# Optimization experiments

Measured on AMD Instinct MI355X. Metric: run time of the kernel, lower is better.

Reference implementation:

```python
import jax, jax.numpy as jnp
import numpy as np

KERNEL_SIZE = 5
SIGMA = 2.0
HALF_K = KERNEL_SIZE // 2


def _gaussian_kernel():
    # torch: arange(-k//2+1, k//2+1) with python floor div -> [-2,...,2] for k=5
    ax = jnp.arange(-(KERNEL_SIZE // 2), KERNEL_SIZE // 2 + 1, dtype=jnp.float32)
    xx, yy = jnp.meshgrid(ax, ax, indexing='ij')
    k = jnp.exp(-(xx ** 2 + yy ** 2) / (2.0 * SIGMA ** 2))
    return k / k.sum()  # [5,5]


def setup_inputs() -> dict:
    key = jax.random.key(0)
    k1, k2 = jax.random.split(key)
    feature_map = jax.random.normal(k1, (512, 256, 256), dtype=jnp.float32)
    keypoints = jax.random.randint(k2, (4096, 2), 0, 256, dtype=jnp.int64)
    return {"feature_map": feature_map, "keypoints": keypoints}


def reference(feature_map, keypoints):
    C, H, W = feature_map.shape
    kern = _gaussian_kernel().astype(feature_map.dtype)  # [5,5]
    x = jnp.clip(keypoints[:, 0].astype(jnp.int32), HALF_K, W - HALF_K - 1)  # [N]
    y = jnp.clip(keypoints[:, 1].astype(jnp.int32), HALF_K, H - HALF_K - 1)  # [N]

    def pool_one(xi, yi):
        patch = jax.lax.dynamic_slice(
            feature_map, (0, yi - HALF_K, xi - HALF_K), (C, KERNEL_SIZE, KERNEL_SIZE)
        )  # [C,5,5]
        return jnp.einsum('chw,hw->c', patch, kern)  # [C]

    return jax.vmap(pool_one)(x, y)  # [N,C]
```

## Files before the change

kernel.cpp:

```cpp
#include <hip/hip_runtime.h>


#define NC  512
#define NH  256
#define NW  256
#define NKP 4096

#define OCT 8
#define SLICE_ROWS 36
#define STR 260

#define WS_LIST_OFF_I 16
#define WS_OUTT_OFF_B 262144

__global__ __launch_bounds__(256) void bucket_kernel(
    const int* __restrict__ kp, unsigned* __restrict__ ws_i, int n_kp)
{
    __shared__ unsigned llist[NKP];
    __shared__ int lcnt;
    const int q = blockIdx.x;
    const int t = threadIdx.x;
    if (t == 0) lcnt = 0;
    __syncthreads();

    for (int i = t; i < n_kp; i += 256) {
        int x = kp[2 * i + 0];
        int y = kp[2 * i + 1];
        x = min(max(x, 2), NW - 3);
        y = min(max(y, 2), NH - 3);
        if ((y >> 5) == q) {
            int pos = atomicAdd(&lcnt, 1);
            llist[pos] = (unsigned)i | ((unsigned)x << 12) | ((unsigned)y << 20);
        }
    }
    __syncthreads();
    const int c = lcnt;
    for (int i = t; i < c; i += 256)
        ws_i[WS_LIST_OFF_I + q * NKP + i] = llist[i];
    if (t == 0) ws_i[q] = (unsigned)c;
}

__global__ __launch_bounds__(256) void pool_kernel(
    const float* __restrict__ fm, const unsigned* __restrict__ ws_i,
    float* __restrict__ outT)
{
    __shared__ float plane[SLICE_ROWS * STR];

    const int c = blockIdx.x;
    const int q = blockIdx.y;
    const int t = threadIdx.x;
    const int ybase = q * 32 - 2;

    const float4* src = (const float4*)(fm + ((size_t)c << 16));
#pragma unroll
    for (int it = 0; it < (SLICE_ROWS * 64) / 256; ++it) {
        const int i = t + it * 256;
        const int row = i >> 6;
        const int col4 = i & 63;
        const int gr = ybase + row;
        if ((unsigned)gr < 256u) {
            float4 v = src[(gr << 6) + col4];
            *(float4*)&plane[row * STR + (col4 << 2)] = v;
        }
    }
    __syncthreads();

    const float e1 = 0.8824969025845955f;
    const float e2 = 0.6065306597126334f;
    const float s  = 2.0f * (e1 + e2) + 1.0f;
    const float inv_s2 = 1.0f / (s * s);
    const float g[5] = {e2, e1, 1.0f, e1, e2};
    float gy[5];
#pragma unroll
    for (int i = 0; i < 5; i++) gy[i] = g[i] * inv_s2;

    const int cnt = (int)ws_i[q];
    const unsigned* list = ws_i + WS_LIST_OFF_I + q * NKP;

    for (int e = t; e < cnt; e += 256) {
        const unsigned pk = list[e];
        const int n  = (int)(pk & 0xFFFu);
        const int xc = (int)((pk >> 12) & 0xFFu);
        const int yc = (int)((pk >> 20) & 0xFFu);

        const int x0 = xc - 2;
        const int r  = x0 & 3;
        const int xa = x0 - r;
        float wx[8];
#pragma unroll
        for (int i = 0; i < 8; i++)
            wx[i] = (i >= r && i < r + 5) ? g[i - r] : 0.0f;

        const int lr0 = yc - (q << 5);
        float acc = 0.0f;
#pragma unroll
        for (int dy = 0; dy < 5; dy++) {
            const float* rowp = &plane[(lr0 + dy) * STR + xa];
            float4 a = *(const float4*)rowp;
            float4 b = *(const float4*)(rowp + 4);
            acc += gy[dy] * (a.x * wx[0] + a.y * wx[1] + a.z * wx[2] + a.w * wx[3]
                           + b.x * wx[4] + b.y * wx[5] + b.z * wx[6] + b.w * wx[7]);
        }
        outT[((size_t)c << 12) + n] = acc;
    }
}

__global__ __launch_bounds__(256) void outt_kernel(
    const float* __restrict__ outT, float* __restrict__ out)
{
    __shared__ float tile[32][33];
    const int n0 = blockIdx.x * 32;
    const int c0 = blockIdx.y * 32;
    const int tx = threadIdx.x;
    const int ty = threadIdx.y;

#pragma unroll
    for (int k = 0; k < 32; k += 8)
        tile[ty + k][tx] = outT[(size_t)(c0 + ty + k) * NKP + n0 + tx];
    __syncthreads();
#pragma unroll
    for (int k = 0; k < 32; k += 8)
        out[(size_t)(n0 + ty + k) * NC + c0 + tx] = tile[tx][ty + k];
}

__global__ __launch_bounds__(256) void gpool_direct_kernel(
    const float* __restrict__ fm, const int* __restrict__ kp,
    float* __restrict__ out)
{
    const int n = blockIdx.x;
    const int t = threadIdx.x;

    int x = kp[2 * n + 0];
    int y = kp[2 * n + 1];
    x = min(max(x, 2), NW - 3);
    y = min(max(y, 2), NH - 3);

    const float e1 = 0.8824969025845955f;
    const float e2 = 0.6065306597126334f;
    const float s  = 2.0f * (e1 + e2) + 1.0f;
    const float inv_s2 = 1.0f / (s * s);
    float g[5] = {e2, e1, 1.0f, e1, e2};
    float gy[5];
#pragma unroll
    for (int i = 0; i < 5; i++) gy[i] = g[i] * inv_s2;

    const int x0 = x - 2;
    const int r  = x0 & 3;
    const int xa = x0 - r;
    float wx[8];
#pragma unroll
    for (int i = 0; i < 8; i++)
        wx[i] = (i >= r && i < r + 5) ? g[i - r] : 0.0f;

    const float* base0 = fm + ((size_t)t * NH + (y - 2)) * NW + xa;
    const float* base1 = fm + ((size_t)(t + 256) * NH + (y - 2)) * NW + xa;

    float acc0 = 0.0f, acc1 = 0.0f;
#pragma unroll
    for (int dy = 0; dy < 5; dy++) {
        const float4* p0 = (const float4*)(base0 + dy * NW);
        const float4* p1 = (const float4*)(base1 + dy * NW);
        float4 a0 = p0[0], b0 = p0[1], a1 = p1[0], b1 = p1[1];
        acc0 += gy[dy] * (a0.x * wx[0] + a0.y * wx[1] + a0.z * wx[2] + a0.w * wx[3]
                        + b0.x * wx[4] + b0.y * wx[5] + b0.z * wx[6] + b0.w * wx[7]);
        acc1 += gy[dy] * (a1.x * wx[0] + a1.y * wx[1] + a1.z * wx[2] + a1.w * wx[3]
                        + b1.x * wx[4] + b1.y * wx[5] + b1.z * wx[6] + b1.w * wx[7]);
    }

    out[(size_t)n * NC + t]       = acc0;
    out[(size_t)n * NC + t + 256] = acc1;
}

extern "C" void kernel_launch(void* const* d_in, const int* in_sizes, int n_in,
                              void* d_out, int out_size, void* d_ws, size_t ws_size,
                              hipStream_t stream)
{
    const float* fm  = (const float*)d_in[0];
    const int*   kp  = (const int*)d_in[1];
    float*       out = (float*)d_out;
    const int n_kp   = in_sizes[1] / 2;

    const size_t need = WS_OUTT_OFF_B + (size_t)NC * NKP * sizeof(float);
    if (ws_size >= need && n_kp == NKP) {
        unsigned* ws_i = (unsigned*)d_ws;
        float* outT    = (float*)((char*)d_ws + WS_OUTT_OFF_B);

        bucket_kernel<<<OCT, 256, 0, stream>>>(kp, ws_i, n_kp);

        dim3 pgrid(NC, OCT);
        pool_kernel<<<pgrid, 256, 0, stream>>>(fm, ws_i, outT);

        dim3 tgrid(NKP / 32, NC / 32);
        dim3 tblk(32, 8);
        outt_kernel<<<tgrid, tblk, 0, stream>>>(outT, out);
    } else {
        gpool_direct_kernel<<<n_kp, 256, 0, stream>>>(fm, kp, out);
    }
}
```

Measured before the change: 219.0 us.

## Write pooled results contiguously per bucket and gather via position map in transpose

The bucketing kernel now uses a single wavefront with ballot/popcount ranking, so the list order is deterministic and matches keypoint order. It also records each keypoint's slot position. The pool kernel writes its results contiguously per bucket instead of scattering them by keypoint index. The transpose kernel then gathers through the position map. This turns the pool kernel's scattered stores into coalesced ones, at the cost of an 8x larger intermediate buffer (mostly unused) and gathered reads in the transpose.

```diff
diff --git a/kernel.cpp b/kernel.cpp
--- a/kernel.cpp
+++ b/kernel.cpp
@@ -9,35 +9,40 @@
 #define OCT 8
 #define SLICE_ROWS 36
 #define STR 260
-
-#define WS_LIST_OFF_I 16
+#define OTSTRIDE (OCT * NKP)
+
+#define WS_POS_OFF_I  16
+#define WS_LIST_OFF_I 8192
 #define WS_OUTT_OFF_B 262144
 
-__global__ __launch_bounds__(256) void bucket_kernel(
+__global__ __launch_bounds__(64) void bucket_kernel(
     const int* __restrict__ kp, unsigned* __restrict__ ws_i, int n_kp)
 {
-    __shared__ unsigned llist[NKP];
-    __shared__ int lcnt;
-    const int q = blockIdx.x;
-    const int t = threadIdx.x;
-    if (t == 0) lcnt = 0;
-    __syncthreads();
-
-    for (int i = t; i < n_kp; i += 256) {
-        int x = kp[2 * i + 0];
-        int y = kp[2 * i + 1];
-        x = min(max(x, 2), NW - 3);
-        y = min(max(y, 2), NH - 3);
-        if ((y >> 5) == q) {
-            int pos = atomicAdd(&lcnt, 1);
-            llist[pos] = (unsigned)i | ((unsigned)x << 12) | ((unsigned)y << 20);
-        }
-    }
-    __syncthreads();
-    const int c = lcnt;
-    for (int i = t; i < c; i += 256)
-        ws_i[WS_LIST_OFF_I + q * NKP + i] = llist[i];
-    if (t == 0) ws_i[q] = (unsigned)c;
+    const int q    = blockIdx.x;
+    const int lane = threadIdx.x;
+    int base = 0;
+    for (int i0 = 0; i0 < n_kp; i0 += 64) {
+        const int i = i0 + lane;
+        int x = 0, y = 0;
+        bool in = false;
+        if (i < n_kp) {
+            x = kp[2 * i + 0];
+            y = kp[2 * i + 1];
+            x = min(max(x, 2), NW - 3);
+            y = min(max(y, 2), NH - 3);
+            in = ((y >> 5) == q);
+        }
+        const unsigned long long m = __ballot(in);
+        const int rank = __popcll(m & ((1ull << lane) - 1ull));
+        if (in) {
+            const int slot = base + rank;
+            ws_i[WS_LIST_OFF_I + q * NKP + slot] =
+                (unsigned)i | ((unsigned)x << 12) | ((unsigned)y << 20);
+            ws_i[WS_POS_OFF_I + i] = (unsigned)(q * NKP + slot);
+        }
+        base += __popcll(m);
+    }
+    if (lane == 0) ws_i[q] = (unsigned)base;
 }
 
 __global__ __launch_bounds__(256) void pool_kernel(
@@ -76,10 +81,10 @@
 
     const int cnt = (int)ws_i[q];
     const unsigned* list = ws_i + WS_LIST_OFF_I + q * NKP;
+    float* orow = outT + (size_t)c * OTSTRIDE + q * NKP;
 
     for (int e = t; e < cnt; e += 256) {
         const unsigned pk = list[e];
-        const int n  = (int)(pk & 0xFFFu);
         const int xc = (int)((pk >> 12) & 0xFFu);
         const int yc = (int)((pk >> 20) & 0xFFu);
 
@@ -101,22 +106,27 @@
             acc += gy[dy] * (a.x * wx[0] + a.y * wx[1] + a.z * wx[2] + a.w * wx[3]
                            + b.x * wx[4] + b.y * wx[5] + b.z * wx[6] + b.w * wx[7]);
         }
-        outT[((size_t)c << 12) + n] = acc;
+        orow[e] = acc;
     }
 }
 
 __global__ __launch_bounds__(256) void outt_kernel(
-    const float* __restrict__ outT, float* __restrict__ out)
+    const float* __restrict__ outT, const unsigned* __restrict__ ws_i,
+    float* __restrict__ out)
 {
     __shared__ float tile[32][33];
+    __shared__ unsigned pos_s[32];
     const int n0 = blockIdx.x * 32;
     const int c0 = blockIdx.y * 32;
     const int tx = threadIdx.x;
     const int ty = threadIdx.y;
 
+    if (ty == 0) pos_s[tx] = ws_i[WS_POS_OFF_I + n0 + tx];
+    __syncthreads();
+
 #pragma unroll
     for (int k = 0; k < 32; k += 8)
-        tile[ty + k][tx] = outT[(size_t)(c0 + ty + k) * NKP + n0 + tx];
+        tile[ty + k][tx] = outT[(size_t)(c0 + ty + k) * OTSTRIDE + pos_s[tx]];
     __syncthreads();
 #pragma unroll
     for (int k = 0; k < 32; k += 8)
@@ -180,19 +190,19 @@
     float*       out = (float*)d_out;
     const int n_kp   = in_sizes[1] / 2;
 
-    const size_t need = WS_OUTT_OFF_B + (size_t)NC * NKP * sizeof(float);
+    const size_t need = WS_OUTT_OFF_B + (size_t)NC * OTSTRIDE * sizeof(float);
     if (ws_size >= need && n_kp == NKP) {
         unsigned* ws_i = (unsigned*)d_ws;
         float* outT    = (float*)((char*)d_ws + WS_OUTT_OFF_B);
 
-        bucket_kernel<<<OCT, 256, 0, stream>>>(kp, ws_i, n_kp);
+        bucket_kernel<<<OCT, 64, 0, stream>>>(kp, ws_i, n_kp);
 
         dim3 pgrid(NC, OCT);
         pool_kernel<<<pgrid, 256, 0, stream>>>(fm, ws_i, outT);
 
         dim3 tgrid(NKP / 32, NC / 32);
         dim3 tblk(32, 8);
-        outt_kernel<<<tgrid, tblk, 0, stream>>>(outT, out);
+        outt_kernel<<<tgrid, tblk, 0, stream>>>(outT, ws_i, out);
     } else {
         gpool_direct_kernel<<<n_kp, 256, 0, stream>>>(fm, kp, out);
     }
```

Measured after the change: 241.9 us. +10.5%, slower.

## Parallelize keypoint bucketing, drop transpose kernel, write output directly

Applied to the files above, without the earlier changes.

The bucketing kernel now runs across many blocks, using a shared histogram and global atomics on per-band counters that a memset zeroes first. The pool kernel uses 512-thread blocks and writes results straight into the [N,C] output, so the intermediate outT buffer and the separate transpose kernel are gone. This saves a full write and read of the 8 MB intermediate plus one launch. The cost is strided, uncoalesced scattered stores to out, since adjacent threads write different keypoints for the same channel.

```diff
diff --git a/kernel.cpp b/kernel.cpp
--- a/kernel.cpp
+++ b/kernel.cpp
@@ -10,39 +10,43 @@
 #define SLICE_ROWS 36
 #define STR 260
 
-#define WS_LIST_OFF_I 16
-#define WS_OUTT_OFF_B 262144
+#define WS_LIST_OFF_I 8192
 
 __global__ __launch_bounds__(256) void bucket_kernel(
     const int* __restrict__ kp, unsigned* __restrict__ ws_i, int n_kp)
 {
-    __shared__ unsigned llist[NKP];
-    __shared__ int lcnt;
-    const int q = blockIdx.x;
+    __shared__ int hist[OCT];
+    __shared__ int base[OCT];
     const int t = threadIdx.x;
-    if (t == 0) lcnt = 0;
+    const int i = blockIdx.x * 256 + t;
+
+    if (t < OCT) hist[t] = 0;
     __syncthreads();
 
-    for (int i = t; i < n_kp; i += 256) {
+    int q = 0, lr = 0;
+    unsigned pk = 0;
+    const bool valid = (i < n_kp);
+    if (valid) {
         int x = kp[2 * i + 0];
         int y = kp[2 * i + 1];
         x = min(max(x, 2), NW - 3);
         y = min(max(y, 2), NH - 3);
-        if ((y >> 5) == q) {
-            int pos = atomicAdd(&lcnt, 1);
-            llist[pos] = (unsigned)i | ((unsigned)x << 12) | ((unsigned)y << 20);
-        }
+        q  = y >> 5;
+        lr = atomicAdd(&hist[q], 1);
+        pk = (unsigned)i | ((unsigned)x << 12) | ((unsigned)y << 20);
     }
     __syncthreads();
-    const int c = lcnt;
-    for (int i = t; i < c; i += 256)
-        ws_i[WS_LIST_OFF_I + q * NKP + i] = llist[i];
-    if (t == 0) ws_i[q] = (unsigned)c;
+
+    if (t < OCT) base[t] = atomicAdd((int*)&ws_i[t], hist[t]);
+    __syncthreads();
+
+    if (valid)
+        ws_i[WS_LIST_OFF_I + q * NKP + base[q] + lr] = pk;
 }
 
-__global__ __launch_bounds__(256) void pool_kernel(
+__global__ __launch_bounds__(512) void pool_kernel(
     const float* __restrict__ fm, const unsigned* __restrict__ ws_i,
-    float* __restrict__ outT)
+    float* __restrict__ out)
 {
     __shared__ float plane[SLICE_ROWS * STR];
 
@@ -53,14 +57,16 @@
 
     const float4* src = (const float4*)(fm + ((size_t)c << 16));
 #pragma unroll
-    for (int it = 0; it < (SLICE_ROWS * 64) / 256; ++it) {
-        const int i = t + it * 256;
-        const int row = i >> 6;
-        const int col4 = i & 63;
-        const int gr = ybase + row;
-        if ((unsigned)gr < 256u) {
-            float4 v = src[(gr << 6) + col4];
-            *(float4*)&plane[row * STR + (col4 << 2)] = v;
+    for (int it = 0; it < 5; ++it) {
+        const int i = t + it * 512;
+        if (i < SLICE_ROWS * 64) {
+            const int row  = i >> 6;
+            const int col4 = i & 63;
+            const int gr   = ybase + row;
+            if ((unsigned)gr < 256u) {
+                float4 v = src[(gr << 6) + col4];
+                *(float4*)&plane[row * STR + (col4 << 2)] = v;
+            }
         }
     }
     __syncthreads();
@@ -77,7 +83,7 @@
     const int cnt = (int)ws_i[q];
     const unsigned* list = ws_i + WS_LIST_OFF_I + q * NKP;
 
-    for (int e = t; e < cnt; e += 256) {
+    for (int e = t; e < cnt; e += 512) {
         const unsigned pk = list[e];
         const int n  = (int)(pk & 0xFFFu);
         const int xc = (int)((pk >> 12) & 0xFFu);
@@ -101,26 +107,8 @@
             acc += gy[dy] * (a.x * wx[0] + a.y * wx[1] + a.z * wx[2] + a.w * wx[3]
                            + b.x * wx[4] + b.y * wx[5] + b.z * wx[6] + b.w * wx[7]);
         }
-        outT[((size_t)c << 12) + n] = acc;
+        out[(size_t)n * NC + c] = acc;
     }
-}
-
-__global__ __launch_bounds__(256) void outt_kernel(
-    const float* __restrict__ outT, float* __restrict__ out)
-{
-    __shared__ float tile[32][33];
-    const int n0 = blockIdx.x * 32;
-    const int c0 = blockIdx.y * 32;
-    const int tx = threadIdx.x;
-    const int ty = threadIdx.y;
-
-#pragma unroll
-    for (int k = 0; k < 32; k += 8)
-        tile[ty + k][tx] = outT[(size_t)(c0 + ty + k) * NKP + n0 + tx];
-    __syncthreads();
-#pragma unroll
-    for (int k = 0; k < 32; k += 8)
-        out[(size_t)(n0 + ty + k) * NC + c0 + tx] = tile[tx][ty + k];
 }
 
 __global__ __launch_bounds__(256) void gpool_direct_kernel(
@@ -180,19 +168,16 @@
     float*       out = (float*)d_out;
     const int n_kp   = in_sizes[1] / 2;
 
-    const size_t need = WS_OUTT_OFF_B + (size_t)NC * NKP * sizeof(float);
+    const size_t need = (WS_LIST_OFF_I + (size_t)OCT * NKP) * sizeof(unsigned);
     if (ws_size >= need && n_kp == NKP) {
         unsigned* ws_i = (unsigned*)d_ws;
-        float* outT    = (float*)((char*)d_ws + WS_OUTT_OFF_B);
 
-        bucket_kernel<<<OCT, 256, 0, stream>>>(kp, ws_i, n_kp);
+        hipMemsetAsync(d_ws, 0, OCT * sizeof(unsigned), stream);
+
+        bucket_kernel<<<(NKP + 255) / 256, 256, 0, stream>>>(kp, ws_i, n_kp);
 
         dim3 pgrid(NC, OCT);
-        pool_kernel<<<pgrid, 256, 0, stream>>>(fm, ws_i, outT);
-
-        dim3 tgrid(NKP / 32, NC / 32);
-        dim3 tblk(32, 8);
-        outt_kernel<<<tgrid, tblk, 0, stream>>>(outT, out);
+        pool_kernel<<<pgrid, 512, 0, stream>>>(fm, ws_i, out);
     } else {
         gpool_direct_kernel<<<n_kp, 256, 0, stream>>>(fm, kp, out);
     }
```

Result: faster. 210.7 us (-3.8%).
